# Kernel tuning notes

Hardware: AMD Instinct MI355X
Metric: run time of the kernel (lower is better)

## Reference

```python
import jax, jax.numpy as jnp
import numpy as np

B, S, HID = 2, 2048, 2048
H, D = 16, 128
BASE = 10000.0
NEG = -1e9


def _rope_tables(seq_len, dim, dtype):
    inv_freq = 1.0 / (BASE ** (jnp.arange(0, dim, 2, dtype=jnp.float32) / dim))
    pos = jnp.arange(seq_len, dtype=jnp.float32)
    freqs = jnp.einsum('s,d->sd', pos, inv_freq)          # [S, D/2]
    emb = jnp.concatenate([freqs, freqs], axis=-1)        # [S, D]
    return jnp.cos(emb).astype(dtype), jnp.sin(emb).astype(dtype)


def _rotate_half(x):
    x1, x2 = jnp.split(x, 2, axis=-1)
    return jnp.concatenate([-x2, x1], axis=-1)


def setup_inputs() -> dict:
    key = jax.random.key(0)
    k1, k2, k3 = jax.random.split(key, 3)
    x = jax.random.normal(k1, (B, S, HID), dtype=jnp.float32)
    w_qkv = jax.random.normal(k2, (HID, 3 * HID), dtype=jnp.float32) * (HID ** -0.5)
    w_out = jax.random.normal(k3, (HID, HID), dtype=jnp.float32) * (HID ** -0.5)
    return {"x": x, "w_qkv": w_qkv, "w_out": w_out}


def reference(x, w_qkv, w_out):
    b, s, _ = x.shape
    qkv = x @ w_qkv                                        # [B, S, 3*HID]
    qkv = qkv.reshape(b, s, 3, H, D).transpose(2, 0, 3, 1, 4)  # [3, B, H, S, D]
    q, k, v = qkv[0], qkv[1], qkv[2]
    cos, sin = _rope_tables(s, D, x.dtype)                 # [S, D]
    cos = cos[None, None]
    sin = sin[None, None]
    q = q * cos + _rotate_half(q) * sin
    k = k * cos + _rotate_half(k) * sin
    scale = 1.0 / np.sqrt(D)
    scores = jnp.einsum('bhqd,bhkd->bhqk', q, k) * scale   # [B, H, S, S]
    causal = jnp.triu(jnp.ones((s, s), dtype=bool), k=1)
    scores = jnp.where(causal[None, None], NEG, scores)
    attn = jax.nn.softmax(scores, axis=-1)
    out = jnp.einsum('bhqk,bhkd->bhqd', attn, v)           # [B, H, S, D]
    out = out.transpose(0, 2, 1, 3).reshape(b, s, H * D)
    return out @ w_out
```

## Files before the change

### kernel.cpp

```cpp
#include <hip/hip_runtime.h>
#include <hip/hip_bf16.h>

#define S_LEN 2048
#define HID_DIM 2048
#define NH 16
#define HD 128
#define N3 6144

typedef __bf16 bf16x8 __attribute__((ext_vector_type(8)));
typedef unsigned short u16x8 __attribute__((ext_vector_type(8)));
typedef float f32x4 __attribute__((ext_vector_type(4)));
typedef float f32x16 __attribute__((ext_vector_type(16)));

#define MFMA16(a, b, c) __builtin_amdgcn_mfma_f32_16x16x32_bf16(a, b, c, 0, 0, 0)
#define MFMA32(a, b, c) __builtin_amdgcn_mfma_f32_32x32x16_bf16(a, b, c, 0, 0, 0)

__device__ __forceinline__ unsigned short f2bf(float f) {
  union { float f; unsigned u; } v; v.f = f;
  return (unsigned short)((v.u + 0x7fffu + ((v.u >> 16) & 1u)) >> 16);
}
__device__ __forceinline__ float bf2f(unsigned short h) {
  union { unsigned u; float f; } v; v.u = ((unsigned)h) << 16; return v.f;
}
__device__ __forceinline__ unsigned packbf2(float lo, float hi) {
  union { __hip_bfloat162 h2; unsigned u; } cv;
  cv.h2 = __float22bfloat162_rn(make_float2(lo, hi));
  return cv.u;
}
__device__ __forceinline__ void store_c(float* p, float v) { *p = v; }
__device__ __forceinline__ void store_c(unsigned short* p, float v) { *p = f2bf(v); }

__device__ __forceinline__ float fexp2(float x) {
  float r; asm("v_exp_f32 %0, %1" : "=v"(r) : "v"(x)); return r;
}

__device__ __forceinline__ void async16(const void* g, void* l) {
  __builtin_amdgcn_global_load_lds((const __attribute__((address_space(1))) unsigned int*)g,
                                   (__attribute__((address_space(3))) unsigned int*)l,
                                   16, 0, 0);
}

template <int N> __device__ __forceinline__ void vmcnt();
template <> __device__ __forceinline__ void vmcnt<0>() { asm volatile("s_waitcnt vmcnt(0)" ::: "memory"); }
template <> __device__ __forceinline__ void vmcnt<5>() { asm volatile("s_waitcnt vmcnt(5)" ::: "memory"); }
template <> __device__ __forceinline__ void vmcnt<6>() { asm volatile("s_waitcnt vmcnt(6)" ::: "memory"); }

#define PLSWAP(a, b) asm volatile("v_permlane32_swap_b32 %0, %1" : "+v"(a), "+v"(b))

__global__ __launch_bounds__(256) void prep_all(const float4* __restrict__ x4,
                                                ushort4* __restrict__ xb4,
                                                const float* __restrict__ w_qkv,
                                                unsigned short* __restrict__ wqkvT,
                                                const float* __restrict__ w_out,
                                                unsigned short* __restrict__ woutT,
                                                float* __restrict__ cosT,
                                                float* __restrict__ sinT) {
  __shared__ float t[32][33];
  int bid = blockIdx.x;
  const int tid = threadIdx.x;

  if (bid < 8192) {
    int i = bid * 256 + tid;
    float4 v = x4[i];
    ushort4 o;
    o.x = f2bf(v.x); o.y = f2bf(v.y); o.z = f2bf(v.z); o.w = f2bf(v.w);
    xb4[i] = o;
    return;
  }
  bid -= 8192;
  if (bid < 12288 + 4096) {
    const float* src; unsigned short* dst; int R, Ccols;
    if (bid < 12288) { src = w_qkv; dst = wqkvT; R = 2048; Ccols = 6144; }
    else { bid -= 12288; src = w_out; dst = woutT; R = 2048; Ccols = 2048; }
    int ct = Ccols >> 5;
    int bx = bid % ct, by = bid / ct;
    int c0 = bx << 5, r0 = by << 5;
    int lx = tid & 31, ly = tid >> 5;
#pragma unroll
    for (int i = 0; i < 32; i += 8)
      t[ly + i][lx] = src[(long long)(r0 + ly + i) * Ccols + c0 + lx];
    __syncthreads();
    {
      const int j = tid >> 3;
      const int seg = tid & 7;
      ushort4 o;
      o.x = f2bf(t[seg * 4 + 0][j]);
      o.y = f2bf(t[seg * 4 + 1][j]);
      o.z = f2bf(t[seg * 4 + 2][j]);
      o.w = f2bf(t[seg * 4 + 3][j]);
      *(ushort4*)(dst + (long long)(c0 + j) * R + r0 + seg * 4) = o;
    }
    return;
  }
  bid -= 16384;
  int idx = bid * 256 + tid;
  int s = idx >> 6, i = idx & 63;
  float invf = powf(10000.0f, -(float)i * (1.0f / 64.0f));
  float a = (float)s * invf;
  cosT[idx] = cosf(a);
  sinT[idx] = sinf(a);
}

__global__ __launch_bounds__(512) void gemm256(const unsigned short* __restrict__ A,
                                               const unsigned short* __restrict__ Bt,
                                               unsigned short* __restrict__ C,
                                               int Mdim, int Ncols, int ldc, int Kdim) {
  constexpr int AEL = 256 * 64, BUFE = 2 * AEL;
  __shared__ unsigned short smem[2 * BUFE];

  const int ntn = Ncols >> 8;
  const int nwg = (Mdim >> 8) * ntn;
  int bid = blockIdx.x;
  bid = (bid & 7) * (nwg >> 3) + (bid >> 3);
  const int tm = (bid / ntn) << 8;
  const int tn = (bid % ntn) << 8;

  const int tid = threadIdx.x;
  const int w = tid >> 6, l = tid & 63;
  const int g = l >> 4, cc = l & 15;
  const int wm = w >> 2, wn = w & 3;

  const int srow = tid >> 3;
  const int schunk = (tid & 7) ^ (srow & 7);
  const unsigned short* gA = A + (long long)(tm + srow) * Kdim + schunk * 8;
  const unsigned short* gB = Bt + (long long)(tn + srow) * Kdim + schunk * 8;

  const int ch0 = ((g) ^ (cc & 7)) << 3;
  const int ch1 = ((4 + g) ^ (cc & 7)) << 3;

  f32x4 acc[8][4] = {};
  bf16x8 a[4][2], b[4][2];
  const int nk = Kdim >> 6;

#define ST_A(kt2, BUF, s) \
  async16(gA + (long long)(s) * 64 * Kdim + ((long long)(kt2) << 6), \
          smem + (BUF) * BUFE + (s) * 4096 + w * 512)
#define ST_B(kt2, BUF, s) \
  async16(gB + (long long)(s) * 64 * Kdim + ((long long)(kt2) << 6), \
          smem + (BUF) * BUFE + AEL + (s) * 4096 + w * 512)

#pragma unroll
  for (int s = 0; s < 4; ++s) ST_A(0, 0, s);
#pragma unroll
  for (int s = 0; s < 4; ++s) ST_B(0, 0, s);
  ST_A(1, 1, 0); ST_A(1, 1, 2);
  ST_B(1, 1, 0); ST_B(1, 1, 1); ST_B(1, 1, 2); ST_B(1, 1, 3);
  vmcnt<6>();
  __builtin_amdgcn_s_barrier();

#define KSTEP(kt, BUF, OBUF)                                                      \
  {                                                                               \
    const unsigned short* Ab = smem + (BUF) * BUFE + wm * (128 * 64);             \
    const unsigned short* Bb = smem + (BUF) * BUFE + AEL + wn * (64 * 64);        \
                    \
    _Pragma("unroll") for (int i = 0; i < 4; ++i) {                               \
      const int r = (i * 16 + cc) << 6;                                           \
      a[i][0] = *(const bf16x8*)(Ab + r + ch0);                                   \
      a[i][1] = *(const bf16x8*)(Ab + r + ch1);                                   \
    }                                                                             \
    _Pragma("unroll") for (int j = 0; j < 2; ++j) {                               \
      const int r = (j * 16 + cc) << 6;                                           \
      b[j][0] = *(const bf16x8*)(Bb + r + ch0);                                   \
      b[j][1] = *(const bf16x8*)(Bb + r + ch1);                                   \
    }                                                                             \
    if ((kt) + 1 < nk) { ST_A((kt) + 1, OBUF, 1); ST_A((kt) + 1, OBUF, 3); }      \
    __builtin_amdgcn_s_barrier();                                                 \
    __builtin_amdgcn_s_setprio(1);                                                \
    _Pragma("unroll") for (int i = 0; i < 4; ++i)                                 \
      _Pragma("unroll") for (int j = 0; j < 2; ++j) {                             \
        acc[i][j] = MFMA16(a[i][0], b[j][0], acc[i][j]);                          \
        acc[i][j] = MFMA16(a[i][1], b[j][1], acc[i][j]);                          \
      }                                                                           \
    __builtin_amdgcn_s_setprio(0);                                                \
    __builtin_amdgcn_s_barrier();                                                 \
                                              \
    _Pragma("unroll") for (int j = 0; j < 2; ++j) {                               \
      const int r = ((2 + j) * 16 + cc) << 6;                                     \
      b[2 + j][0] = *(const bf16x8*)(Bb + r + ch0);                               \
      b[2 + j][1] = *(const bf16x8*)(Bb + r + ch1);                               \
    }                                                                             \
    if ((kt) + 2 < nk) { ST_A((kt) + 2, BUF, 0); ST_A((kt) + 2, BUF, 2); }        \
    __builtin_amdgcn_s_barrier();                                                 \
    __builtin_amdgcn_s_setprio(1);                                                \
    _Pragma("unroll") for (int i = 0; i < 4; ++i)                                 \
      _Pragma("unroll") for (int j = 0; j < 2; ++j) {                             \
        acc[i][2 + j] = MFMA16(a[i][0], b[2 + j][0], acc[i][2 + j]);              \
        acc[i][2 + j] = MFMA16(a[i][1], b[2 + j][1], acc[i][2 + j]);              \
      }                                                                           \
    __builtin_amdgcn_s_setprio(0);                                                \
    __builtin_amdgcn_s_barrier();                                                 \
                                              \
    _Pragma("unroll") for (int i = 0; i < 4; ++i) {                               \
      const int r = ((64 + i * 16 + cc) << 6);                                    \
      a[i][0] = *(const bf16x8*)(Ab + r + ch0);                                   \
      a[i][1] = *(const bf16x8*)(Ab + r + ch1);                                   \
    }                                                                             \
    if ((kt) + 2 < nk) { ST_B((kt) + 2, BUF, 0); ST_B((kt) + 2, BUF, 1); }        \
    __builtin_amdgcn_s_barrier();                                                 \
    __builtin_amdgcn_s_setprio(1);                                                \
    _Pragma("unroll") for (int i = 0; i < 4; ++i)                                 \
      _Pragma("unroll") for (int j = 0; j < 2; ++j) {                             \
        acc[4 + i][j] = MFMA16(a[i][0], b[j][0], acc[4 + i][j]);                  \
        acc[4 + i][j] = MFMA16(a[i][1], b[j][1], acc[4 + i][j]);                  \
      }                                                                           \
    __builtin_amdgcn_s_setprio(0);                                                \
    __builtin_amdgcn_s_barrier();                                                 \
                            \
    if ((kt) + 2 < nk) { ST_B((kt) + 2, BUF, 2); ST_B((kt) + 2, BUF, 3); }        \
    __builtin_amdgcn_s_barrier();                                                 \
    __builtin_amdgcn_s_setprio(1);                                                \
    _Pragma("unroll") for (int i = 0; i < 4; ++i)                                 \
      _Pragma("unroll") for (int j = 0; j < 2; ++j) {                             \
        acc[4 + i][2 + j] = MFMA16(a[i][0], b[2 + j][0], acc[4 + i][2 + j]);      \
        acc[4 + i][2 + j] = MFMA16(a[i][1], b[2 + j][1], acc[4 + i][2 + j]);      \
      }                                                                           \
    __builtin_amdgcn_s_setprio(0);                                                \
    if ((kt) + 2 < nk) vmcnt<6>(); else vmcnt<0>();                               \
    __builtin_amdgcn_s_barrier();                                                 \
  }

  for (int kt = 0; kt < nk; kt += 2) {
    KSTEP(kt, 0, 1);
    KSTEP(kt + 1, 1, 0);
  }
#undef KSTEP
#undef ST_A
#undef ST_B

  const int crow0 = tm + wm * 128;
  const int ccol0 = tn + wn * 64;
#pragma unroll
  for (int i = 0; i < 8; ++i)
#pragma unroll
    for (int j = 0; j < 4; ++j)
#pragma unroll
      for (int p = 0; p < 4; ++p) {
        int row = crow0 + i * 16 + (g << 2) + p;
        int col = ccol0 + j * 16 + cc;
        store_c(&C[(long long)row * ldc + col], acc[i][j][p]);
      }
}

template <int BM, int BN, typename OutT, bool VTOUT = false>
__global__ __launch_bounds__(512) void gemm_pipe8(const unsigned short* __restrict__ A,
                                                  const unsigned short* __restrict__ Bt,
                                                  OutT* __restrict__ C,
                                                  int Mdim, int Ncols, int ldc, int Kdim) {
  constexpr int WTM = BM / 2, WTN = BN / 4;
  constexpr int MREP = WTM / 16, NREP = WTN / 16;
  constexpr int AEL = BM * 64, BEL = BN * 64, BUFE = AEL + BEL;
  constexpr int AINST = BM / 64, BINST = BN / 64;
  constexpr int AHALF = BM / 128, BHALF = BN / 128;
  constexpr int VN = BN / 64 + BM / 128;
  __shared__ unsigned short smem[2 * BUFE];

  const int ntn = Ncols / BN;
  const int nwg = (Mdim / BM) * ntn;
  int bid = blockIdx.x;
  bid = (bid & 7) * (nwg >> 3) + (bid >> 3);
  const int tm = (bid / ntn) * BM;
  const int tn = (bid % ntn) * BN;

  const int tid = threadIdx.x;
  const int w = tid >> 6, l = tid & 63;
  const int g = l >> 4, cc = l & 15;
  const int wm = w >> 2, wn = w & 3;

  const int srow = tid >> 3;
  const int schunk = (tid & 7) ^ (srow & 7);
  const unsigned short* gA = A + (long long)(tm + srow) * Kdim + schunk * 8;
  const unsigned short* gB = Bt + (long long)(tn + srow) * Kdim + schunk * 8;

  const int ch0 = ((g) ^ (cc & 7)) << 3;
  const int ch1 = ((4 + g) ^ (cc & 7)) << 3;

  f32x4 acc[MREP][NREP] = {};
  bf16x8 a[MREP / 2][2], b[NREP][2];

  const int nk = Kdim >> 6;

#define STAGE_A(kt2, s) \
  async16(gA + (long long)(s) * 64 * Kdim + ((long long)(kt2) << 6), \
          smem + ((kt2) & 1) * BUFE + (s) * 4096 + w * 512)
#define STAGE_B(kt2, s) \
  async16(gB + (long long)(s) * 64 * Kdim + ((long long)(kt2) << 6), \
          smem + ((kt2) & 1) * BUFE + AEL + (s) * 4096 + w * 512)

#pragma unroll
  for (int s = 0; s < AINST; ++s) STAGE_A(0, s);
#pragma unroll
  for (int s = 0; s < BINST; ++s) STAGE_B(0, s);
#pragma unroll
  for (int s = 0; s < BINST; ++s) STAGE_B(1, s);
#pragma unroll
  for (int s = 0; s < AHALF; ++s) STAGE_A(1, s);
  vmcnt<VN>();
  __builtin_amdgcn_s_barrier();

  for (int kt = 0; kt < nk; ++kt) {
    const int buf = kt & 1;
    const unsigned short* Ab = smem + buf * BUFE + (wm * WTM) * 64;
    const unsigned short* Bb = smem + buf * BUFE + AEL + (wn * WTN) * 64;

#pragma unroll
    for (int i = 0; i < MREP / 2; ++i) {
      const int r = (i * 16 + cc) << 6;
      a[i][0] = *(const bf16x8*)(Ab + r + ch0);
      a[i][1] = *(const bf16x8*)(Ab + r + ch1);
    }
#pragma unroll
    for (int j = 0; j < NREP; ++j) {
      const int r = (j * 16 + cc) << 6;
      b[j][0] = *(const bf16x8*)(Bb + r + ch0);
      b[j][1] = *(const bf16x8*)(Bb + r + ch1);
    }
    if (kt + 1 < nk) {
#pragma unroll
      for (int s = AHALF; s < AINST; ++s) STAGE_A(kt + 1, s);
    }
    __builtin_amdgcn_s_barrier();
    __builtin_amdgcn_s_setprio(1);
#pragma unroll
    for (int i = 0; i < MREP / 2; ++i)
#pragma unroll
      for (int j = 0; j < NREP / 2; ++j) {
        acc[i][j] = MFMA16(a[i][0], b[j][0], acc[i][j]);
        acc[i][j] = MFMA16(a[i][1], b[j][1], acc[i][j]);
      }
    __builtin_amdgcn_s_setprio(0);
    __builtin_amdgcn_s_barrier();

    if (kt + 2 < nk) {
#pragma unroll
      for (int s = 0; s < BHALF; ++s) STAGE_B(kt + 2, s);
    }
    __builtin_amdgcn_s_barrier();
    __builtin_amdgcn_s_setprio(1);
#pragma unroll
    for (int i = 0; i < MREP / 2; ++i)
#pragma unroll
      for (int j = 0; j < NREP / 2; ++j) {
        f32x4& ac = acc[i][NREP / 2 + j];
        ac = MFMA16(a[i][0], b[NREP / 2 + j][0], ac);
        ac = MFMA16(a[i][1], b[NREP / 2 + j][1], ac);
      }
    __builtin_amdgcn_s_setprio(0);
    __builtin_amdgcn_s_barrier();

#pragma unroll
    for (int i = 0; i < MREP / 2; ++i) {
      const int r = ((WTM / 2) + i * 16 + cc) << 6;
      a[i][0] = *(const bf16x8*)(Ab + r + ch0);
      a[i][1] = *(const bf16x8*)(Ab + r + ch1);
    }
    if (kt + 2 < nk) {
#pragma unroll
      for (int s = BHALF; s < BINST; ++s) STAGE_B(kt + 2, s);
    }
    __builtin_amdgcn_s_barrier();
    __builtin_amdgcn_s_setprio(1);
#pragma unroll
    for (int i = 0; i < MREP / 2; ++i)
#pragma unroll
      for (int j = 0; j < NREP / 2; ++j) {
        f32x4& ac = acc[MREP / 2 + i][j];
        ac = MFMA16(a[i][0], b[j][0], ac);
        ac = MFMA16(a[i][1], b[j][1], ac);
      }
    __builtin_amdgcn_s_setprio(0);
    __builtin_amdgcn_s_barrier();

    if (kt + 2 < nk) {
#pragma unroll
      for (int s = 0; s < AHALF; ++s) STAGE_A(kt + 2, s);
    }
    __builtin_amdgcn_s_barrier();
    __builtin_amdgcn_s_setprio(1);
#pragma unroll
    for (int i = 0; i < MREP / 2; ++i)
#pragma unroll
      for (int j = 0; j < NREP / 2; ++j) {
        f32x4& ac = acc[MREP / 2 + i][NREP / 2 + j];
        ac = MFMA16(a[i][0], b[NREP / 2 + j][0], ac);
        ac = MFMA16(a[i][1], b[NREP / 2 + j][1], ac);
      }
    __builtin_amdgcn_s_setprio(0);
    if (kt + 2 < nk) vmcnt<VN>(); else vmcnt<0>();
    __builtin_amdgcn_s_barrier();
  }
#undef STAGE_A
#undef STAGE_B

  const int crow0 = tm + wm * WTM;
  const int ccol0 = tn + wn * WTN;
  if constexpr (VTOUT) {
    unsigned short* Vt = (unsigned short*)C;
#pragma unroll
    for (int i = 0; i < MREP; ++i)
#pragma unroll
      for (int j = 0; j < NREP; ++j) {
        int col = ccol0 + j * 16 + cc;
        int rowb = crow0 + i * 16 + (g << 2);
        long long vt = ((long long)(((rowb >> 11) << 4) + (col >> 7)) * 128 + (col & 127)) * 2048 +
                       (rowb & 2047);
        ushort4 o;
        o.x = f2bf(acc[i][j][0]); o.y = f2bf(acc[i][j][1]);
        o.z = f2bf(acc[i][j][2]); o.w = f2bf(acc[i][j][3]);
        *(ushort4*)(Vt + vt) = o;
      }
  } else {
#pragma unroll
    for (int i = 0; i < MREP; ++i)
#pragma unroll
      for (int j = 0; j < NREP; ++j)
#pragma unroll
        for (int p = 0; p < 4; ++p) {
          int row = crow0 + i * 16 + (g << 2) + p;
          int col = ccol0 + j * 16 + cc;
          store_c(&C[(long long)row * ldc + col], acc[i][j][p]);
        }
  }
}

__global__ __launch_bounds__(256) void split_rope(const unsigned short* __restrict__ qkv,
                                                  const float* __restrict__ cosT,
                                                  const float* __restrict__ sinT,
                                                  unsigned short* __restrict__ Qb,
                                                  unsigned short* __restrict__ Kb) {
  const int bid = blockIdx.x;
  const int st = bid & 63;
  const int h = (bid >> 6) & 15;
  const int b = bid >> 10;
  const int s0 = st << 5;
  const int t = threadIdx.x;
  const float qscale = 0.08838834764831845f * 1.4426950408889634f;

  const int sl = t >> 3;
  const int d0 = (t & 7) << 3;
  const int s = s0 + sl;
  const long long rb = ((long long)(b * S_LEN + s)) * N3 + h * HD;
  u16x8 qlo = *(const u16x8*)(qkv + rb + d0);
  u16x8 qhi = *(const u16x8*)(qkv + rb + 64 + d0);
  u16x8 klo = *(const u16x8*)(qkv + rb + HID_DIM + d0);
  u16x8 khi = *(const u16x8*)(qkv + rb + HID_DIM + 64 + d0);
  const float* cp = cosT + (s << 6) + d0;
  const float* sp = sinT + (s << 6) + d0;
  f32x4 c0 = *(const f32x4*)(cp), c1 = *(const f32x4*)(cp + 4);
  f32x4 sn0 = *(const f32x4*)(sp), sn1 = *(const f32x4*)(sp + 4);
  u16x8 qo_lo, qo_hi, ko_lo, ko_hi;
#pragma unroll
  for (int j = 0; j < 8; ++j) {
    float cv = (j < 4) ? c0[j & 3] : c1[j & 3];
    float sv = (j < 4) ? sn0[j & 3] : sn1[j & 3];
    float ql = bf2f(qlo[j]), qh = bf2f(qhi[j]);
    float kl = bf2f(klo[j]), kh = bf2f(khi[j]);
    qo_lo[j] = f2bf((ql * cv - qh * sv) * qscale);
    qo_hi[j] = f2bf((qh * cv + ql * sv) * qscale);
    ko_lo[j] = f2bf(kl * cv - kh * sv);
    ko_hi[j] = f2bf(kh * cv + kl * sv);
  }
  const long long ob = ((long long)((b * NH + h) * S_LEN + s)) * HD + d0;
  *(u16x8*)(Qb + ob) = qo_lo;
  *(u16x8*)(Qb + ob + 64) = qo_hi;
  *(u16x8*)(Kb + ob) = ko_lo;
  *(u16x8*)(Kb + ob + 64) = ko_hi;
}

__global__ __launch_bounds__(256) void flash_attn(const unsigned short* __restrict__ Qg,
                                                  const unsigned short* __restrict__ Kg,
                                                  const unsigned short* __restrict__ Vt,
                                                  unsigned short* __restrict__ Ob) {
  __shared__ unsigned short smem[32768];
  const int id = blockIdx.x;
  const int bh = id & 31;
  const int qtr = (id >> 5) & 7;
  const int qt = (id >> 8) ? qtr : 15 - qtr;
  const int Q0 = qt << 7;
  const int b = bh >> 4, h = bh & 15;
  const long long base = (long long)bh * (S_LEN * HD);
  const int tid = threadIdx.x, w = tid >> 6, l = tid & 63;
  const int hi = l >> 5, q = l & 31;
  const int q0w = Q0 + (w << 5);
  const int g = l >> 4, c = l & 15;

  bf16x8 qf[8];
  {
    const unsigned short* qp = Qg + base + (long long)(q0w + q) * HD + (hi << 3);
#pragma unroll
    for (int s = 0; s < 8; ++s) qf[s] = *(const bf16x8*)(qp + (s << 4));
  }

  f32x16 oacc[4] = {};
  float m = -1e30f, lsum = 0.f;

  const int nt = (qt << 1) + 2;

  auto STAGE = [&](int kv0, int buf) {
    unsigned short* ks = smem + buf * 8192;
    unsigned short* vs = smem + 16384 + buf * 8192;
#pragma unroll
    for (int j = 0; j < 4; ++j) {
      int row = (w << 4) + (j << 2) + g;
      int chunk = c ^ (row & 15);
      async16(Kg + base + (long long)(kv0 + row) * HD + (chunk << 3),
              ks + (((w << 4) + (j << 2)) << 7));
    }
#pragma unroll
    for (int j = 0; j < 4; ++j) {
      int dr = (w << 5) + (j << 3) + (l >> 3);
      int chunk = (l & 7) ^ (dr & 7);
      async16(Vt + base + (long long)dr * S_LEN + kv0 + (chunk << 3),
              vs + (((w << 5) + (j << 3)) << 6));
    }
  };

  STAGE(0, 0);
  __syncthreads();

  int cur = 0;
  for (int t = 0; t < nt; ++t) {
    const int kv0 = t << 6;
    if (t + 1 < nt) STAGE((t + 1) << 6, cur ^ 1);

    if (kv0 < q0w + 32) {
      const unsigned short* ks = smem + cur * 8192;
      const unsigned short* vs = smem + 16384 + cur * 8192;

      f32x16 sa[2] = {};
#pragma unroll
      for (int h2 = 0; h2 < 2; ++h2) {
        const char* kb = (const char*)ks + (((h2 << 5) + q) << 8);
        const int rm = q & 15;
#pragma unroll
        for (int s = 0; s < 8; ++s) {
          bf16x8 kf = *(const bf16x8*)(kb + ((((s << 1) + hi) ^ rm) << 4));
          sa[h2] = MFMA32(kf, qf[s], sa[h2]);
        }
      }

      if (kv0 + 63 > q0w) {
        const int qq = q0w + q;
#pragma unroll
        for (int h2 = 0; h2 < 2; ++h2)
#pragma unroll
          for (int j = 0; j < 16; ++j) {
            int kv = kv0 + (h2 << 5) + (j & 3) + ((j >> 2) << 3) + (hi << 2);
            if (kv > qq) sa[h2][j] = -1e30f;
          }
      }

      float t0 = sa[0][0], t1 = sa[0][1], t2 = sa[0][2], t3 = sa[0][3];
#pragma unroll
      for (int j = 4; j < 16; j += 4) {
        t0 = fmaxf(t0, sa[0][j]);     t1 = fmaxf(t1, sa[0][j + 1]);
        t2 = fmaxf(t2, sa[0][j + 2]); t3 = fmaxf(t3, sa[0][j + 3]);
      }
#pragma unroll
      for (int j = 0; j < 16; j += 4) {
        t0 = fmaxf(t0, sa[1][j]);     t1 = fmaxf(t1, sa[1][j + 1]);
        t2 = fmaxf(t2, sa[1][j + 2]); t3 = fmaxf(t3, sa[1][j + 3]);
      }
      float tmax = fmaxf(fmaxf(t0, t1), fmaxf(t2, t3));
      {
        float tcp;
        asm volatile("v_mov_b32 %0, %1" : "=v"(tcp) : "v"(tmax));
        PLSWAP(tmax, tcp);
        tmax = fmaxf(tmax, tcp);
      }
      float mn = fmaxf(m, tmax);
      float fsc = fexp2(m - mn);
      m = mn;
      float s0 = 0.f, s1 = 0.f, s2 = 0.f, s3 = 0.f;
#pragma unroll
      for (int h2 = 0; h2 < 2; ++h2)
#pragma unroll
        for (int j = 0; j < 16; j += 4) {
          float p0 = fexp2(sa[h2][j] - mn);
          float p1 = fexp2(sa[h2][j + 1] - mn);
          float p2 = fexp2(sa[h2][j + 2] - mn);
          float p3 = fexp2(sa[h2][j + 3] - mn);
          sa[h2][j] = p0; sa[h2][j + 1] = p1;
          sa[h2][j + 2] = p2; sa[h2][j + 3] = p3;
          s0 += p0; s1 += p1; s2 += p2; s3 += p3;
        }
      float ps = (s0 + s1) + (s2 + s3);
      {
        float pcp;
        asm volatile("v_mov_b32 %0, %1" : "=v"(pcp) : "v"(ps));
        PLSWAP(ps, pcp);
        ps = ps + pcp;
      }
      lsum = lsum * fsc + ps;
#pragma unroll
      for (int db = 0; db < 4; ++db)
#pragma unroll
        for (int j = 0; j < 16; ++j) oacc[db][j] *= fsc;

      unsigned up[2][8];
#pragma unroll
      for (int h2 = 0; h2 < 2; ++h2)
#pragma unroll
        for (int k = 0; k < 8; ++k)
          up[h2][k] = packbf2(sa[h2][2 * k], sa[h2][2 * k + 1]);
      union Frag { unsigned u[4]; bf16x8 v; } pf[4];
#pragma unroll
      for (int s = 0; s < 4; ++s) {
        int h2 = s >> 1, q4 = (s & 1) << 2;
        unsigned a0 = up[h2][q4 + 0], b0 = up[h2][q4 + 2];
        unsigned a1 = up[h2][q4 + 1], b1 = up[h2][q4 + 3];
        PLSWAP(a0, b0);
        PLSWAP(a1, b1);
        pf[s].u[0] = a0; pf[s].u[1] = a1;
        pf[s].u[2] = b0; pf[s].u[3] = b1;
      }

#pragma unroll
      for (int db = 0; db < 4; ++db) {
        const char* vb = (const char*)vs + (((db << 5) + q) << 7);
        const int d7 = q & 7;
#pragma unroll
        for (int s = 0; s < 4; ++s) {
          bf16x8 vf = *(const bf16x8*)(vb + ((((s << 1) + hi) ^ d7) << 4));
          oacc[db] = MFMA32(vf, pf[s].v, oacc[db]);
        }
      }
    }

    __syncthreads();
    cur ^= 1;
  }

  const float rl = 1.0f / lsum;
#pragma unroll
  for (int db = 0; db < 4; ++db)
#pragma unroll
    for (int jg = 0; jg < 4; ++jg) {
      int d = (db << 5) + (jg << 3) + (hi << 2);
      unsigned v0 = packbf2(oacc[db][4 * jg] * rl, oacc[db][4 * jg + 1] * rl);
      unsigned v1 = packbf2(oacc[db][4 * jg + 2] * rl, oacc[db][4 * jg + 3] * rl);
      *(uint2*)(smem + (((w << 5) + q) << 7) + d) = make_uint2(v0, v1);
    }
  __syncthreads();
  {
    const int qr = tid >> 1;
    const int dh = (tid & 1) << 6;
    const uint4* src = (const uint4*)(smem + (qr << 7) + dh);
    uint4* dst = (uint4*)(Ob + (long long)((b << 11) + Q0 + qr) * HID_DIM + (h << 7) + dh);
#pragma unroll
    for (int cc2 = 0; cc2 < 8; ++cc2) dst[cc2] = src[cc2];
  }
}

extern "C" void kernel_launch(void* const* d_in, const int* in_sizes, int n_in,
                              void* d_out, int out_size, void* d_ws, size_t ws_size,
                              hipStream_t stream) {
  (void)in_sizes; (void)n_in; (void)out_size; (void)ws_size;
  const float* x = (const float*)d_in[0];
  const float* w_qkv = (const float*)d_in[1];
  const float* w_out = (const float*)d_in[2];
  float* out = (float*)d_out;
  char* ws = (char*)d_ws;

  unsigned short* xb    = (unsigned short*)(ws);
  unsigned short* wqkvT = (unsigned short*)(ws + 16777216);
  unsigned short* woutT = (unsigned short*)(ws + 41943040);
  unsigned short* qkv   = (unsigned short*)(ws + 50331648);
  unsigned short* Qb    = (unsigned short*)(ws + 100663296);
  unsigned short* Kb    = (unsigned short*)(ws + 117440512);
  unsigned short* Vt    = (unsigned short*)(ws + 134217728);
  float* cosT = (float*)(ws + 150994944);
  float* sinT = (float*)(ws + 151519232);
  unsigned short* Ob = qkv;

  prep_all<<<25088, 256, 0, stream>>>((const float4*)x, (ushort4*)xb,
                                      w_qkv, wqkvT, w_out, woutT, cosT, sinT);
  gemm256<<<256, 512, 0, stream>>>(xb, wqkvT, qkv, 4096, 4096, 6144, 2048);
  gemm_pipe8<128, 256, unsigned short, true><<<256, 512, 0, stream>>>(
      xb, wqkvT + (long long)4096 * 2048, Vt, 4096, 2048, 2048, 2048);
  split_rope<<<2048, 256, 0, stream>>>(qkv, cosT, sinT, Qb, Kb);
  flash_attn<<<512, 256, 0, stream>>>(Qb, Kb, Vt, Ob);
  gemm_pipe8<128, 256, float><<<256, 512, 0, stream>>>(Ob, woutT, out, 4096, 2048, 2048, 2048);
}
```

Baseline: 259.4 us.

## Fuse RoPE and Q/K head split into QK projection GEMM epilogue

Removes the separate split_rope kernel. The QK GEMM epilogue now stages its bf16 accumulator tile in shared memory, one half at a time. It then applies rotary embedding (plus the softmax scale for Q) and writes directly into head-major Q and K buffers. This drops a full write and reread of the Q/K portion of the qkv intermediate and one kernel launch. The cost is extra LDS traffic and barriers in the GEMM epilogue.

```diff
diff --git a/kernel.cpp b/kernel.cpp
--- a/kernel.cpp
+++ b/kernel.cpp
@@ -101,10 +101,13 @@
   sinT[idx] = sinf(a);
 }
 
-__global__ __launch_bounds__(512) void gemm256(const unsigned short* __restrict__ A,
-                                               const unsigned short* __restrict__ Bt,
-                                               unsigned short* __restrict__ C,
-                                               int Mdim, int Ncols, int ldc, int Kdim) {
+__global__ __launch_bounds__(512) void gemm256_rope(const unsigned short* __restrict__ A,
+                                                    const unsigned short* __restrict__ Bt,
+                                                    unsigned short* __restrict__ Qb,
+                                                    unsigned short* __restrict__ Kb,
+                                                    const float* __restrict__ cosT,
+                                                    const float* __restrict__ sinT,
+                                                    int Mdim, int Ncols, int Kdim) {
   constexpr int AEL = 256 * 64, BUFE = 2 * AEL;
   __shared__ unsigned short smem[2 * BUFE];
 
@@ -227,18 +230,53 @@
 #undef ST_A
 #undef ST_B
 
-  const int crow0 = tm + wm * 128;
-  const int ccol0 = tn + wn * 64;
-#pragma unroll
-  for (int i = 0; i < 8; ++i)
-#pragma unroll
-    for (int j = 0; j < 4; ++j)
-#pragma unroll
-      for (int p = 0; p < 4; ++p) {
-        int row = crow0 + i * 16 + (g << 2) + p;
-        int col = ccol0 + j * 16 + cc;
-        store_c(&C[(long long)row * ldc + col], acc[i][j][p]);
-      }
+  const bool isQ = tn < 2048;
+  unsigned short* qkout = isQ ? Qb : Kb;
+  const float scl = isQ ? (0.08838834764831845f * 1.4426950408889634f) : 1.0f;
+  const int colbase = tn & 2047;
+  __syncthreads();
+#pragma unroll
+  for (int pass = 0; pass < 2; ++pass) {
+    if (wm == pass) {
+#pragma unroll
+      for (int i = 0; i < 8; ++i)
+#pragma unroll
+        for (int j = 0; j < 4; ++j)
+#pragma unroll
+          for (int p = 0; p < 4; ++p)
+            smem[(i * 16 + (g << 2) + p) * 264 + wn * 64 + j * 16 + cc] = f2bf(acc[i][j][p]);
+    }
+    __syncthreads();
+    {
+      const int r = tid >> 2;
+      const int c0 = (tid & 3) << 6;
+      const int grow = tm + (pass << 7) + r;
+      const int bb = grow >> 11, ss = grow & 2047;
+      const float* cpb = cosT + (ss << 6);
+      const float* spb = sinT + (ss << 6);
+#pragma unroll
+      for (int k2 = 0; k2 < 8; ++k2) {
+        const int c = c0 + (k2 << 3);
+        const int gcol = colbase + c;
+        const int hh = gcol >> 7, dd = gcol & 127;
+        u16x8 v = *(const u16x8*)(smem + r * 264 + c);
+        u16x8 pr = *(const u16x8*)(smem + r * 264 + (c ^ 64));
+        const int d6 = dd & 63;
+        f32x4 ca = *(const f32x4*)(cpb + d6), cb = *(const f32x4*)(cpb + d6 + 4);
+        f32x4 sa4 = *(const f32x4*)(spb + d6), sb4 = *(const f32x4*)(spb + d6 + 4);
+        const float sgn = (dd < 64) ? -1.0f : 1.0f;
+        u16x8 o;
+#pragma unroll
+        for (int e = 0; e < 8; ++e) {
+          float cv = (e < 4) ? ca[e & 3] : cb[e & 3];
+          float sv = (e < 4) ? sa4[e & 3] : sb4[e & 3];
+          o[e] = f2bf((bf2f(v[e]) * cv + sgn * bf2f(pr[e]) * sv) * scl);
+        }
+        *(u16x8*)(qkout + ((long long)((bb * NH + hh) * S_LEN + ss) * HD + dd)) = o;
+      }
+    }
+    __syncthreads();
+  }
 }
 
 template <int BM, int BN, typename OutT, bool VTOUT = false>
@@ -420,50 +458,6 @@
           store_c(&C[(long long)row * ldc + col], acc[i][j][p]);
         }
   }
-}
-
-__global__ __launch_bounds__(256) void split_rope(const unsigned short* __restrict__ qkv,
-                                                  const float* __restrict__ cosT,
-                                                  const float* __restrict__ sinT,
-                                                  unsigned short* __restrict__ Qb,
-                                                  unsigned short* __restrict__ Kb) {
-  const int bid = blockIdx.x;
-  const int st = bid & 63;
-  const int h = (bid >> 6) & 15;
-  const int b = bid >> 10;
-  const int s0 = st << 5;
-  const int t = threadIdx.x;
-  const float qscale = 0.08838834764831845f * 1.4426950408889634f;
-
-  const int sl = t >> 3;
-  const int d0 = (t & 7) << 3;
-  const int s = s0 + sl;
-  const long long rb = ((long long)(b * S_LEN + s)) * N3 + h * HD;
-  u16x8 qlo = *(const u16x8*)(qkv + rb + d0);
-  u16x8 qhi = *(const u16x8*)(qkv + rb + 64 + d0);
-  u16x8 klo = *(const u16x8*)(qkv + rb + HID_DIM + d0);
-  u16x8 khi = *(const u16x8*)(qkv + rb + HID_DIM + 64 + d0);
-  const float* cp = cosT + (s << 6) + d0;
-  const float* sp = sinT + (s << 6) + d0;
-  f32x4 c0 = *(const f32x4*)(cp), c1 = *(const f32x4*)(cp + 4);
-  f32x4 sn0 = *(const f32x4*)(sp), sn1 = *(const f32x4*)(sp + 4);
-  u16x8 qo_lo, qo_hi, ko_lo, ko_hi;
-#pragma unroll
-  for (int j = 0; j < 8; ++j) {
-    float cv = (j < 4) ? c0[j & 3] : c1[j & 3];
-    float sv = (j < 4) ? sn0[j & 3] : sn1[j & 3];
-    float ql = bf2f(qlo[j]), qh = bf2f(qhi[j]);
-    float kl = bf2f(klo[j]), kh = bf2f(khi[j]);
-    qo_lo[j] = f2bf((ql * cv - qh * sv) * qscale);
-    qo_hi[j] = f2bf((qh * cv + ql * sv) * qscale);
-    ko_lo[j] = f2bf(kl * cv - kh * sv);
-    ko_hi[j] = f2bf(kh * cv + kl * sv);
-  }
-  const long long ob = ((long long)((b * NH + h) * S_LEN + s)) * HD + d0;
-  *(u16x8*)(Qb + ob) = qo_lo;
-  *(u16x8*)(Qb + ob + 64) = qo_hi;
-  *(u16x8*)(Kb + ob) = ko_lo;
-  *(u16x8*)(Kb + ob + 64) = ko_hi;
 }
 
 __global__ __launch_bounds__(256) void flash_attn(const unsigned short* __restrict__ Qg,
@@ -674,10 +668,9 @@
 
   prep_all<<<25088, 256, 0, stream>>>((const float4*)x, (ushort4*)xb,
                                       w_qkv, wqkvT, w_out, woutT, cosT, sinT);
-  gemm256<<<256, 512, 0, stream>>>(xb, wqkvT, qkv, 4096, 4096, 6144, 2048);
+  gemm256_rope<<<256, 512, 0, stream>>>(xb, wqkvT, Qb, Kb, cosT, sinT, 4096, 4096, 2048);
   gemm_pipe8<128, 256, unsigned short, true><<<256, 512, 0, stream>>>(
       xb, wqkvT + (long long)4096 * 2048, Vt, 4096, 2048, 2048, 2048);
-  split_rope<<<2048, 256, 0, stream>>>(qkv, cosT, sinT, Qb, Kb);
   flash_attn<<<512, 256, 0, stream>>>(Qb, Kb, Vt, Ob);
   gemm_pipe8<128, 256, float><<<256, 512, 0, stream>>>(Ob, woutT, out, 4096, 2048, 2048, 2048);
 }
```

Result: no change. 254.8 us (-1.8%).
